# Kernel optimization log

Measured on AMD Instinct MI355X. Metric: run time of the kernel, lower is better.

## Reference

```python
import jax, jax.numpy as jnp
import numpy as np


def _l2norm(x, eps=1e-6):
    return x / jnp.sqrt(jnp.sum(x * x, axis=-1, keepdims=True) + eps)


def setup_inputs() -> dict:
    key = jax.random.key(0)
    k1, k2, k3, k4 = jax.random.split(key, 4)
    b, h, L, dk, dv = 2, 8, 4096, 128, 128
    q = jax.random.normal(k1, (b, h, L, dk), jnp.float32)
    k = jax.random.normal(k2, (b, h, L, dk), jnp.float32)
    v = jax.random.normal(k3, (b, h, L, dv), jnp.float32)
    beta = jax.random.uniform(k4, (b, h, L), jnp.float32)  # sigmoid(b_proj) in module -> (0,1)
    return {"q": q, "k": k, "v": v, "beta": beta, "chunk_size": 32}


def _delta_rule_chunkwise(q, k, v, beta, chunk_size):
    b, h, L, dk = q.shape
    dv = v.shape[-1]
    c = chunk_size
    pad = (-L) % c
    if pad:
        q = jnp.pad(q, ((0, 0), (0, 0), (0, pad), (0, 0)))
        k = jnp.pad(k, ((0, 0), (0, 0), (0, pad), (0, 0)))
        v = jnp.pad(v, ((0, 0), (0, 0), (0, pad), (0, 0)))
        beta = jnp.pad(beta, ((0, 0), (0, 0), (0, pad)))
    Lp = L + pad
    n = Lp // c

    q = _l2norm(q)
    k = _l2norm(k)
    v = v * beta[..., None]
    kb = k * beta[..., None]

    # (b,h,n,c,d)
    resh = lambda t: t.reshape(b, h, n, c, t.shape[-1])
    q, k, v, kb = resh(q), resh(k), resh(v), resh(kb)

    tri = jnp.triu(jnp.ones((c, c), bool), 0)        # upper incl diag
    tri_s = jnp.triu(jnp.ones((c, c), bool), 1)      # strict upper

    # forward substitution: inv = (I + strictly-lower(k_beta k^T))^{-1}-style recurrence
    inv = -jnp.einsum('bhncd,bhned->bhnce', kb, k)
    inv = jnp.where(tri, 0.0, inv)
    for i in range(1, c):  # fixed small chunk_size loop (c=32)
        upd = jnp.einsum('bhnk,bhnkj->bhnj', inv[..., i, :], inv[..., :, :i])
        inv = inv.at[..., i, :i].add(upd)
    inv = inv + jnp.eye(c, dtype=inv.dtype)

    u = inv @ v    # (b,h,n,c,dv)
    w = inv @ kb   # (b,h,n,c,dk)

    # chunk-recurrent state scan over the n blocks
    qs = jnp.moveaxis(q, 2, 0)
    ks = jnp.moveaxis(k, 2, 0)
    us = jnp.moveaxis(u, 2, 0)
    ws = jnp.moveaxis(w, 2, 0)
    S0 = jnp.zeros((b, h, dk, dv), q.dtype)

    def step(S, blk):
        q_i, k_i, u_i, w_i = blk
        attn = jnp.einsum('bhcd,bhed->bhce', q_i, k_i)
        attn = jnp.where(tri_s, 0.0, attn)                       # causal within chunk
        u_i = u_i - jnp.einsum('bhcd,bhde->bhce', w_i, S)
        o_i = jnp.einsum('bhcd,bhde->bhce', q_i, S) + jnp.einsum('bhce,bhed->bhcd', attn, u_i)
        S = S + jnp.einsum('bhcd,bhce->bhde', k_i, u_i)
        return S, o_i

    S, out = jax.lax.scan(step, S0, (qs, ks, us, ws))
    out = jnp.moveaxis(out, 0, 2).reshape(b, h, Lp, dv)[:, :, :L]
    return out, S


def reference(q, k, v, beta, chunk_size):
    return _delta_rule_chunkwise(q, k, v, beta, int(chunk_size))
```

## Files before the change

kernel.cpp:

```cpp
#include <hip/hip_runtime.h>
#include <cstddef>

#define BH   16
#define LSEQ 4096
#define DK   128
#define DV   128
#define C    32
#define NCH  128
#define DVB  16
#define NDVB 8
#define PP   136
#define PC   40
#define PS   136
#define AP   33

#define NPLANE (2048u * 4096u)
#define NPLAT  (2048u * 1024u)

typedef __attribute__((ext_vector_type(4))) float f32x4;
typedef __attribute__((ext_vector_type(8))) short short8;
typedef __attribute__((ext_vector_type(4))) short s16x4;

__device__ inline unsigned split_bf16(float x) {
    unsigned u = __builtin_bit_cast(unsigned, x);
    unsigned r = u + 0x7fffu + ((u >> 16) & 1u);
    unsigned h = r >> 16;
    float hf = __builtin_bit_cast(float, r & 0xffff0000u);
    float res = x - hf;
    unsigned u2 = __builtin_bit_cast(unsigned, res);
    unsigned r2 = u2 + 0x7fffu + ((u2 >> 16) & 1u);
    return (h << 16) | (r2 >> 16);
}
__device__ inline short hi_bf16(float x) {
    unsigned u = __builtin_bit_cast(unsigned, x);
    return (short)((u + 0x7fffu + ((u >> 16) & 1u)) >> 16);
}
__device__ inline short trunc_bf16(float x) {
    return (short)(__builtin_bit_cast(unsigned, x) >> 16);
}

__device__ inline short8 fld(const short* P, int row0, int pitch, int k0, int lane) {
    return *(const short8*)(P + (row0 + (lane & 15)) * pitch + k0 + ((lane >> 4) << 3));
}
__device__ inline short8 fldz128(const short* P, int row0, int ks, int lane) {
    int row = row0 + (lane & 15);
    int c = ks * 4 + (lane >> 4);
    return *(const short8*)(P + row * 128 + ((c ^ (row & 7)) << 3));
}
__device__ inline short8 fldz32(const short* P, int row0, int lane) {
    int row = row0 + (lane & 15);
    int c = lane >> 4;
    return *(const short8*)(P + row * 32 + ((c ^ (row & 3)) << 3));
}
__device__ inline f32x4 mf(short8 a, short8 b, f32x4 c) {
    return __builtin_amdgcn_mfma_f32_16x16x32_bf16(a, b, c, 0, 0, 0);
}
__device__ inline void build_ifrags(int lane, short8& Iev, short8& Iod) {
    int n = lane & 15, q = lane >> 4;
#pragma unroll
    for (int j = 0; j < 8; ++j) {
        Iev[j] = (q * 8 + j == n)      ? (short)0x3F80 : (short)0;
        Iod[j] = (q * 8 + j == n + 16) ? (short)0x3F80 : (short)0;
    }
}
__device__ inline void store8_z128(short* Pg, int row, int col0, s16x4 v) {
    int c = col0 >> 3;
    *(s16x4*)(Pg + row * 128 + ((c ^ (row & 7)) << 3) + (col0 & 7)) = v;
}
__device__ inline void store8_z32(short* Pg, int row, int col0, s16x4 v) {
    int c = col0 >> 3;
    *(s16x4*)(Pg + row * 32 + ((c ^ (row & 3)) << 3) + (col0 & 7)) = v;
}
__device__ inline void dma1k(const short* g, short* l, int lane) {
    __builtin_amdgcn_global_load_lds(
        (const __attribute__((address_space(1))) unsigned int*)(g + lane * 8),
        (__attribute__((address_space(3))) unsigned int*)l, 16, 0, 0);
}

__global__ __launch_bounds__(256) void k_prep(const float* __restrict__ Q,
                                              const float* __restrict__ K,
                                              const float* __restrict__ V,
                                              const float* __restrict__ Beta,
                                              short* __restrict__ QHg,
                                              short* __restrict__ WHg,
                                              short* __restrict__ WLg,
                                              short* __restrict__ KTHg,
                                              short* __restrict__ KTLg,
                                              short* __restrict__ ATHg,
                                              short* __restrict__ ATLg,
                                              float* __restrict__ Uws) {
    __shared__ short knh[C * PP], knl[C * PP], vh[C * PP], vl[C * PP], qh[C * PP];
    __shared__ short knTh[DK * PC], knTl[DK * PC], vTh[DK * PC], vTl[DK * PC];
    __shared__ short Th[C * PC], Tl[C * PC];
    __shared__ float A[C * AP];
    __shared__ float sbeta[C];

    const int t = threadIdx.x, lane = t & 63, wv = t >> 6;
    const int quad = (t >> 4) & 3, l15 = t & 15;
    const int g = blockIdx.x;
    const size_t base = (size_t)g * (C * DK);
    short8 Iev, Iod;
    build_ifrags(lane, Iev, Iod);

    if (t < C) sbeta[t] = Beta[(size_t)(g >> 7) * LSEQ + (size_t)(g & 127) * C + t];

    const int sr = t >> 3, sc = (t & 7) * 16;
    f32x4 kk[4], vv[4], qq[4];
#pragma unroll
    for (int g4 = 0; g4 < 4; ++g4) {
        kk[g4] = *(const f32x4*)(K + base + 16 * t + 4 * g4);
        vv[g4] = *(const f32x4*)(V + base + 16 * t + 4 * g4);
        qq[g4] = *(const f32x4*)(Q + base + 16 * t + 4 * g4);
    }
    float ssk = 0.f, ssq = 0.f;
#pragma unroll
    for (int g4 = 0; g4 < 4; ++g4) {
#pragma unroll
        for (int e = 0; e < 4; ++e) {
            ssk += kk[g4][e] * kk[g4][e];
            ssq += qq[g4][e] * qq[g4][e];
        }
    }
    ssk += __shfl_xor(ssk, 1); ssk += __shfl_xor(ssk, 2); ssk += __shfl_xor(ssk, 4);
    ssq += __shfl_xor(ssq, 1); ssq += __shfl_xor(ssq, 2); ssq += __shfl_xor(ssq, 4);
    const float rk = rsqrtf(ssk + 1e-6f), rq = rsqrtf(ssq + 1e-6f);
#pragma unroll
    for (int half = 0; half < 2; ++half) {
        short8 h8, l8;
#pragma unroll
        for (int e = 0; e < 8; ++e) {
            unsigned p = split_bf16(kk[2 * half + (e >> 2)][e & 3] * rk);
            h8[e] = (short)(p >> 16); l8[e] = (short)(p & 0xffffu);
        }
        *(short8*)(knh + sr * PP + sc + 8 * half) = h8;
        *(short8*)(knl + sr * PP + sc + 8 * half) = l8;
#pragma unroll
        for (int e = 0; e < 8; ++e) {
            unsigned p = split_bf16(vv[2 * half + (e >> 2)][e & 3]);
            h8[e] = (short)(p >> 16); l8[e] = (short)(p & 0xffffu);
        }
        *(short8*)(vh + sr * PP + sc + 8 * half) = h8;
        *(short8*)(vl + sr * PP + sc + 8 * half) = l8;
        short8 q8;
#pragma unroll
        for (int e = 0; e < 8; ++e) q8[e] = hi_bf16(qq[2 * half + (e >> 2)][e & 3] * rq);
        *(short8*)(qh + sr * PP + sc + 8 * half) = q8;
        int c = (sc >> 3) + half;
        *(short8*)(QHg + (size_t)g * 4096 + sr * 128 + ((c ^ (sr & 7)) << 3)) = q8;
    }
    __syncthreads();

    if (wv < 3) {
        const int a0 = (wv == 0) ? 0 : 16;
        const int b0 = (wv == 2) ? 16 : 0;
        f32x4 acc = {0.f, 0.f, 0.f, 0.f};
#pragma unroll
        for (int ks = 0; ks < 4; ++ks) {
            short8 ah = fld(knh, a0, PP, ks * 32, lane);
            short8 al = fld(knl, a0, PP, ks * 32, lane);
            short8 bh_ = fld(knh, b0, PP, ks * 32, lane);
            short8 bl_ = fld(knl, b0, PP, ks * 32, lane);
            acc = mf(ah, bh_, mf(ah, bl_, mf(al, bh_, acc)));
        }
#pragma unroll
        for (int r = 0; r < 4; ++r) {
            int row = a0 + quad * 4 + r, col = b0 + l15;
            A[row * AP + col] = (row > col) ? -sbeta[row] * acc[r] : 0.f;
        }
        f32x4 at = {0.f, 0.f, 0.f, 0.f};
#pragma unroll
        for (int ks = 0; ks < 4; ++ks) {
            short8 kh_ = fld(knh, b0, PP, ks * 32, lane);
            short8 kl_ = fld(knl, b0, PP, ks * 32, lane);
            short8 qf = fld(qh, a0, PP, ks * 32, lane);
            at = mf(kh_, qf, mf(kl_, qf, at));
        }
        s16x4 h4, l4;
#pragma unroll
        for (int r = 0; r < 4; ++r) {
            int cj = b0 + quad * 4 + r, ci = a0 + l15;
            float v = (cj <= ci) ? at[r] : 0.f;
            unsigned p = split_bf16(v);
            h4[r] = (short)(p >> 16); l4[r] = (short)(p & 0xffffu);
        }
        store8_z32(ATHg + (size_t)g * 1024, a0 + l15, b0 + quad * 4, h4);
        store8_z32(ATLg + (size_t)g * 1024, a0 + l15, b0 + quad * 4, l4);
    } else {
#pragma unroll
        for (int r = 0; r < 4; ++r) A[l15 * AP + 16 + quad * 4 + r] = 0.f;
        s16x4 z = {0, 0, 0, 0};
        store8_z32(ATHg + (size_t)g * 1024, l15, 16 + quad * 4, z);
        store8_z32(ATLg + (size_t)g * 1024, l15, 16 + quad * 4, z);
    }
    __syncthreads();

    auto tplane = [&](const short* src, short* dst, short* gdst) {
#pragma unroll
        for (int c0 = 0; c0 <= 16; c0 += 16) {
#pragma unroll
            for (int ks = 0; ks < 4; ++ks) {
                short8 fr = fld(src, c0, PP, ks * 32, lane);
                f32x4 z = {0.f, 0.f, 0.f, 0.f};
                f32x4 cA = mf(fr, Iev, z);
                f32x4 cB = mf(fr, Iod, z);
                s16x4 sA, sB;
#pragma unroll
                for (int r = 0; r < 4; ++r) { sA[r] = trunc_bf16(cA[r]); sB[r] = trunc_bf16(cB[r]); }
                *(s16x4*)(dst + (ks * 32 + l15) * PC + c0 + quad * 4) = sA;
                *(s16x4*)(dst + (ks * 32 + 16 + l15) * PC + c0 + quad * 4) = sB;
                if (gdst) {
                    store8_z32(gdst, ks * 32 + l15, c0 + quad * 4, sA);
                    store8_z32(gdst, ks * 32 + 16 + l15, c0 + quad * 4, sB);
                }
            }
        }
    };
    if (wv == 0) {
        tplane(knh, knTh, KTHg + (size_t)g * 4096);
        tplane(vl, vTl, nullptr);
    } else if (wv == 1) {
        tplane(knl, knTl, KTLg + (size_t)g * 4096);
    } else if (wv == 2) {
        tplane(vh, vTh, nullptr);
    } else if (lane < C) {
        const int j = lane;
        for (int i = 1; i < C; ++i) {
            float upd = 0.f;
            for (int kk2 = 1; kk2 < i; ++kk2) upd += A[i * AP + kk2] * A[kk2 * AP + j];
            if (j < i) A[i * AP + j] += upd;
        }
    }
    __syncthreads();

    {
        int tr = t >> 3, tc = (t & 7) * 4;
        s16x4 h4, l4;
#pragma unroll
        for (int e = 0; e < 4; ++e) {
            int j = tc + e;
            float val = ((tr == j) ? 1.f : (tr > j ? A[tr * AP + j] : 0.f)) * sbeta[j];
            unsigned p = split_bf16(val);
            h4[e] = (short)(p >> 16); l4[e] = (short)(p & 0xffffu);
        }
        *(s16x4*)(Th + tr * PC + tc) = h4;
        *(s16x4*)(Tl + tr * PC + tc) = l4;
    }
    __syncthreads();

    {
        const int ci0 = (wv & 1) * 16;
        short8 bTh = fld(Th, ci0, PC, 0, lane);
        short8 bTl = fld(Tl, ci0, PC, 0, lane);
        if (wv < 2) {
#pragma unroll
            for (int tt = 0; tt < 8; ++tt) {
                short8 ah = fld(vTh, tt * 16, PC, 0, lane);
                short8 al = fld(vTl, tt * 16, PC, 0, lane);
                f32x4 z = {0.f, 0.f, 0.f, 0.f};
                f32x4 acc = mf(ah, bTh, mf(ah, bTl, mf(al, bTh, z)));
                *(f32x4*)(Uws + (size_t)g * 4096 + (size_t)(ci0 + l15) * DK + tt * 16 + quad * 4) = acc;
            }
        } else {
#pragma unroll
            for (int tt = 0; tt < 8; ++tt) {
                short8 ah = fld(knTh, tt * 16, PC, 0, lane);
                short8 al = fld(knTl, tt * 16, PC, 0, lane);
                f32x4 z = {0.f, 0.f, 0.f, 0.f};
                f32x4 acc = mf(ah, bTh, mf(ah, bTl, mf(al, bTh, z)));
                s16x4 h4, l4;
#pragma unroll
                for (int r = 0; r < 4; ++r) {
                    unsigned p = split_bf16(acc[r]);
                    h4[r] = (short)(p >> 16); l4[r] = (short)(p & 0xffffu);
                }
                store8_z128(WHg + (size_t)g * 4096, ci0 + l15, tt * 16 + quad * 4, h4);
                store8_z128(WLg + (size_t)g * 4096, ci0 + l15, tt * 16 + quad * 4, l4);
            }
        }
    }
}

__global__ __launch_bounds__(512, 1) void k_scan(const short* __restrict__ QHg,
                                                 const short* __restrict__ WHg,
                                                 const short* __restrict__ WLg,
                                                 const short* __restrict__ KTHg,
                                                 const short* __restrict__ KTLg,
                                                 const short* __restrict__ ATHg,
                                                 const short* __restrict__ ATLg,
                                                 const float* __restrict__ Uws,
                                                 float* __restrict__ Out,
                                                 float* __restrict__ Sout) {
    __shared__ short bQ[2][4096], bWH[2][4096], bWL[2][4096], bKTH[2][4096], bKTL[2][4096];
    __shared__ short bATH[2][1024], bATL[2][1024];
    __shared__ short STh[DVB * PS], STl[DVB * PS];
    __shared__ short uTh[DVB * PC], uTl[DVB * PC];

    const int t = threadIdx.x, lane = t & 63, wv = t >> 6;
    const int quad = (t >> 4) & 3, l15 = t & 15;
    const int db = blockIdx.x >> 4, bhi = blockIdx.x & 15;
    const int vcol = db * DVB;
    const int r0 = (wv & 1) * 16;
    const int dk0 = wv * 16;
    const size_t gb = (size_t)bhi * NCH;

    f32x4 accS = {0.f, 0.f, 0.f, 0.f};
    float pu[4] = {0.f, 0.f, 0.f, 0.f};

    auto dma_chunk = [&](int cc, int s) {
        const size_t go = (gb + cc) * 4096;
        dma1k(QHg + go + wv * 512, &bQ[s][wv * 512], lane);
        dma1k(WHg + go + wv * 512, &bWH[s][wv * 512], lane);
        dma1k(WLg + go + wv * 512, &bWL[s][wv * 512], lane);
        dma1k(KTHg + go + wv * 512, &bKTH[s][wv * 512], lane);
        dma1k(KTLg + go + wv * 512, &bKTL[s][wv * 512], lane);
        if (wv < 4) {
            const size_t ga = (gb + cc) * 1024 + (size_t)(wv & 1) * 512;
            if (wv < 2) dma1k(ATHg + ga, &bATH[s][(wv & 1) * 512], lane);
            else        dma1k(ATLg + ga, &bATL[s][(wv & 1) * 512], lane);
        }
    };
    auto pref_u = [&](int cc) {
        if (wv < 2) {
            const size_t ub = (gb + cc) * 4096;
#pragma unroll
            for (int r = 0; r < 4; ++r)
                pu[r] = Uws[ub + (size_t)(r0 + quad * 4 + r) * DK + vcol + l15];
        }
    };

    for (int e = t; e < DVB * PS; e += 512) { STh[e] = 0; STl[e] = 0; }
    dma_chunk(0, 0);
    pref_u(0);
    __syncthreads();

    for (int cid = 0; cid < NCH; ++cid) {
        const int cur = cid & 1;
        f32x4 oc = {0.f, 0.f, 0.f, 0.f};

        if (wv < 2) {
            f32x4 u0 = {-pu[0], -pu[1], -pu[2], -pu[3]};
            f32x4 u1 = {0.f, 0.f, 0.f, 0.f}, u2 = {0.f, 0.f, 0.f, 0.f};
            f32x4 o1 = {0.f, 0.f, 0.f, 0.f};
#pragma unroll
            for (int ks = 0; ks < 4; ++ks) {
                short8 wh_ = fldz128(bWH[cur], r0, ks, lane);
                short8 wl_ = fldz128(bWL[cur], r0, ks, lane);
                short8 sh_ = fld(STh, 0, PS, ks * 32, lane);
                short8 sl_ = fld(STl, 0, PS, ks * 32, lane);
                short8 qf = fldz128(bQ[cur], r0, ks, lane);
                u0 = mf(wh_, sh_, u0);
                u1 = mf(wh_, sl_, u1);
                u2 = mf(wl_, sh_, u2);
                oc = mf(sh_, qf, oc);
                o1 = mf(sl_, qf, o1);
            }
            oc += o1;
            f32x4 us = u0 + u1 + u2;
            s16x4 h4, l4;
#pragma unroll
            for (int r = 0; r < 4; ++r) {
                unsigned p = split_bf16(-us[r]);
                h4[r] = (short)(p >> 16); l4[r] = (short)(p & 0xffffu);
            }
            *(s16x4*)(uTh + l15 * PC + r0 + quad * 4) = h4;
            *(s16x4*)(uTl + l15 * PC + r0 + quad * 4) = l4;
        }
        __syncthreads();

        short8 buh = fld(uTh, 0, PC, 0, lane);
        short8 bul = fld(uTl, 0, PC, 0, lane);
        if (wv < 2) {
            short8 bah = fldz32(bATH[cur], r0, lane);
            short8 bal = fldz32(bATL[cur], r0, lane);
            oc = mf(buh, bah, mf(buh, bal, mf(bul, bah, oc)));
            const size_t ob = ((size_t)bhi * LSEQ + (size_t)cid * C) * DK;
            *(f32x4*)(Out + ob + (size_t)(r0 + l15) * DK + vcol + quad * 4) = oc;
        }
        {
            short8 kth = fldz32(bKTH[cur], dk0, lane);
            short8 ktl = fldz32(bKTL[cur], dk0, lane);
            f32x4 z = {0.f, 0.f, 0.f, 0.f};
            f32x4 tband = mf(kth, bul, mf(ktl, buh, z));
            accS = mf(kth, buh, accS);
            accS += tband;
            s16x4 h4, l4;
#pragma unroll
            for (int r = 0; r < 4; ++r) {
                unsigned p = split_bf16(accS[r]);
                h4[r] = (short)(p >> 16); l4[r] = (short)(p & 0xffffu);
            }
            *(s16x4*)(STh + l15 * PS + dk0 + quad * 4) = h4;
            *(s16x4*)(STl + l15 * PS + dk0 + quad * 4) = l4;
        }
        if (cid + 1 < NCH) {
            dma_chunk(cid + 1, cur ^ 1);
            pref_u(cid + 1);
        }
        __syncthreads();
    }

#pragma unroll
    for (int r = 0; r < 4; ++r)
        Sout[(size_t)bhi * DK * DV + (size_t)(dk0 + quad * 4 + r) * DV + vcol + l15] = accS[r];
}

extern "C" void kernel_launch(void* const* d_in, const int* in_sizes, int n_in,
                              void* d_out, int out_size, void* d_ws, size_t ws_size,
                              hipStream_t stream) {
    const float* Q    = (const float*)d_in[0];
    const float* K    = (const float*)d_in[1];
    const float* V    = (const float*)d_in[2];
    const float* Beta = (const float*)d_in[3];

    float* Out  = (float*)d_out;
    float* Sout = Out + (size_t)BH * LSEQ * DV;

    short* QHg  = (short*)d_ws;
    short* WHg  = QHg + NPLANE;
    short* WLg  = WHg + NPLANE;
    short* KTHg = WLg + NPLANE;
    short* KTLg = KTHg + NPLANE;
    short* ATHg = KTLg + NPLANE;
    short* ATLg = ATHg + NPLAT;
    float* Uws  = (float*)(ATLg + NPLAT);

    hipLaunchKernelGGL(k_prep, dim3(BH * NCH), dim3(256), 0, stream,
                       Q, K, V, Beta, QHg, WHg, WLg, KTHg, KTLg, ATHg, ATLg, Uws);
    hipLaunchKernelGGL(k_scan, dim3(BH * NDVB), dim3(512), 0, stream,
                       QHg, WHg, WLg, KTHg, KTLg, ATHg, ATLg, Uws, Out, Sout);
}
```

Measured before the change: 356.3 us.

## Issue next-chunk DMA at loop start and defer output stores one iteration

Moves the next chunk's DMA and U prefetch to the start of each iteration so they overlap the current chunk's MFMA work. Output stores are deferred by one chunk, and the U prefetch is double-buffered in registers through a manually unrolled two-chunk loop. __syncthreads is replaced by explicit s_waitcnt plus s_barrier. The aim is to hide global-memory latency behind compute in the serial chunk scan, at the cost of more live registers and a full vmcnt wait at each iteration end.

Result: slower. 373.4 us (+4.8%).

```diff
diff --git a/kernel.cpp b/kernel.cpp
--- a/kernel.cpp
+++ b/kernel.cpp
@@ -304,7 +304,6 @@
     const size_t gb = (size_t)bhi * NCH;
 
     f32x4 accS = {0.f, 0.f, 0.f, 0.f};
-    float pu[4] = {0.f, 0.f, 0.f, 0.f};
 
     auto dma_chunk = [&](int cc, int s) {
         const size_t go = (gb + cc) * 4096;
@@ -319,26 +318,35 @@
             else        dma1k(ATLg + ga, &bATL[s][(wv & 1) * 512], lane);
         }
     };
-    auto pref_u = [&](int cc) {
+    auto pref_u = [&](int cc, f32x4& pn) {
         if (wv < 2) {
             const size_t ub = (gb + cc) * 4096;
 #pragma unroll
             for (int r = 0; r < 4; ++r)
-                pu[r] = Uws[ub + (size_t)(r0 + quad * 4 + r) * DK + vcol + l15];
+                pn[r] = Uws[ub + (size_t)(r0 + quad * 4 + r) * DK + vcol + l15];
         }
     };
 
     for (int e = t; e < DVB * PS; e += 512) { STh[e] = 0; STl[e] = 0; }
+    f32x4 puA = {0.f, 0.f, 0.f, 0.f}, puB = {0.f, 0.f, 0.f, 0.f};
+    f32x4 ocp = {0.f, 0.f, 0.f, 0.f};
     dma_chunk(0, 0);
-    pref_u(0);
+    pref_u(0, puA);
     __syncthreads();
 
-    for (int cid = 0; cid < NCH; ++cid) {
-        const int cur = cid & 1;
+    auto body = [&](int cid, int cur, f32x4& puC, f32x4& puN) {
+        if (wv < 2 && cid > 0) {
+            const size_t ob = ((size_t)bhi * LSEQ + (size_t)(cid - 1) * C) * DK;
+            *(f32x4*)(Out + ob + (size_t)(r0 + l15) * DK + vcol + quad * 4) = ocp;
+        }
+        if (cid + 1 < NCH) {
+            dma_chunk(cid + 1, cur ^ 1);
+            pref_u(cid + 1, puN);
+        }
+
         f32x4 oc = {0.f, 0.f, 0.f, 0.f};
-
         if (wv < 2) {
-            f32x4 u0 = {-pu[0], -pu[1], -pu[2], -pu[3]};
+            f32x4 u0 = {-puC[0], -puC[1], -puC[2], -puC[3]};
             f32x4 u1 = {0.f, 0.f, 0.f, 0.f}, u2 = {0.f, 0.f, 0.f, 0.f};
             f32x4 o1 = {0.f, 0.f, 0.f, 0.f};
 #pragma unroll
@@ -365,7 +373,7 @@
             *(s16x4*)(uTh + l15 * PC + r0 + quad * 4) = h4;
             *(s16x4*)(uTl + l15 * PC + r0 + quad * 4) = l4;
         }
-        __syncthreads();
+        asm volatile("s_waitcnt lgkmcnt(0)\n\ts_barrier" ::: "memory");
 
         short8 buh = fld(uTh, 0, PC, 0, lane);
         short8 bul = fld(uTl, 0, PC, 0, lane);
@@ -373,8 +381,7 @@
             short8 bah = fldz32(bATH[cur], r0, lane);
             short8 bal = fldz32(bATL[cur], r0, lane);
             oc = mf(buh, bah, mf(buh, bal, mf(bul, bah, oc)));
-            const size_t ob = ((size_t)bhi * LSEQ + (size_t)cid * C) * DK;
-            *(f32x4*)(Out + ob + (size_t)(r0 + l15) * DK + vcol + quad * 4) = oc;
+            ocp = oc;
         }
         {
             short8 kth = fldz32(bKTH[cur], dk0, lane);
@@ -392,11 +399,16 @@
             *(s16x4*)(STh + l15 * PS + dk0 + quad * 4) = h4;
             *(s16x4*)(STl + l15 * PS + dk0 + quad * 4) = l4;
         }
-        if (cid + 1 < NCH) {
-            dma_chunk(cid + 1, cur ^ 1);
-            pref_u(cid + 1);
-        }
-        __syncthreads();
+        asm volatile("s_waitcnt vmcnt(0) lgkmcnt(0)\n\ts_barrier" ::: "memory");
+    };
+
+    for (int cp = 0; cp < NCH / 2; ++cp) {
+        body(2 * cp,     0, puA, puB);
+        body(2 * cp + 1, 1, puB, puA);
+    }
+    if (wv < 2) {
+        const size_t ob = ((size_t)bhi * LSEQ + (size_t)(NCH - 1) * C) * DK;
+        *(f32x4*)(Out + ob + (size_t)(r0 + l15) * DK + vcol + quad * 4) = ocp;
     }
 
 #pragma unroll
```

## Pack per-chunk operands into contiguous records and specialize DMA warps in scan

Applied to the files above, without the earlier changes.

Replaces the seven separate global planes (Q, W hi/lo, K^T hi/lo, A^T hi/lo) with one contiguous per-chunk record, so the scan kernel can fetch each chunk as a single linear block into one unified LDS buffer. The next-chunk async copy is now issued at the start of each iteration, and only by the waves that do not compute U/O, so it overlaps with the MFMA work of waves 0-1. K^T and A^T fragment loads are hoisted ahead of the barrier. This gives better locality and earlier prefetch, but all loads land on fewer waves and the scheduling changes.

Result: faster. 339.4 us (-4.8%).

```diff
diff --git a/kernel.cpp b/kernel.cpp
--- a/kernel.cpp
+++ b/kernel.cpp
@@ -14,8 +14,14 @@
 #define PS   136
 #define AP   33
 
-#define NPLANE (2048u * 4096u)
-#define NPLAT  (2048u * 1024u)
+#define RECSZ 22528
+#define OQ    0
+#define OWH   4096
+#define OWL   8192
+#define OKTH  12288
+#define OKTL  16384
+#define OATH  20480
+#define OATL  21504
 
 typedef __attribute__((ext_vector_type(4))) float f32x4;
 typedef __attribute__((ext_vector_type(8))) short short8;
@@ -81,13 +87,7 @@
                                               const float* __restrict__ K,
                                               const float* __restrict__ V,
                                               const float* __restrict__ Beta,
-                                              short* __restrict__ QHg,
-                                              short* __restrict__ WHg,
-                                              short* __restrict__ WLg,
-                                              short* __restrict__ KTHg,
-                                              short* __restrict__ KTLg,
-                                              short* __restrict__ ATHg,
-                                              short* __restrict__ ATLg,
+                                              short* __restrict__ RECg,
                                               float* __restrict__ Uws) {
     __shared__ short knh[C * PP], knl[C * PP], vh[C * PP], vl[C * PP], qh[C * PP];
     __shared__ short knTh[DK * PC], knTl[DK * PC], vTh[DK * PC], vTl[DK * PC];
@@ -99,6 +99,7 @@
     const int quad = (t >> 4) & 3, l15 = t & 15;
     const int g = blockIdx.x;
     const size_t base = (size_t)g * (C * DK);
+    short* rec = RECg + (size_t)g * RECSZ;
     short8 Iev, Iod;
     build_ifrags(lane, Iev, Iod);
 
@@ -146,7 +147,7 @@
         for (int e = 0; e < 8; ++e) q8[e] = hi_bf16(qq[2 * half + (e >> 2)][e & 3] * rq);
         *(short8*)(qh + sr * PP + sc + 8 * half) = q8;
         int c = (sc >> 3) + half;
-        *(short8*)(QHg + (size_t)g * 4096 + sr * 128 + ((c ^ (sr & 7)) << 3)) = q8;
+        *(short8*)(rec + OQ + sr * 128 + ((c ^ (sr & 7)) << 3)) = q8;
     }
     __syncthreads();
 
@@ -183,14 +184,14 @@
             unsigned p = split_bf16(v);
             h4[r] = (short)(p >> 16); l4[r] = (short)(p & 0xffffu);
         }
-        store8_z32(ATHg + (size_t)g * 1024, a0 + l15, b0 + quad * 4, h4);
-        store8_z32(ATLg + (size_t)g * 1024, a0 + l15, b0 + quad * 4, l4);
+        store8_z32(rec + OATH, a0 + l15, b0 + quad * 4, h4);
+        store8_z32(rec + OATL, a0 + l15, b0 + quad * 4, l4);
     } else {
 #pragma unroll
         for (int r = 0; r < 4; ++r) A[l15 * AP + 16 + quad * 4 + r] = 0.f;
         s16x4 z = {0, 0, 0, 0};
-        store8_z32(ATHg + (size_t)g * 1024, l15, 16 + quad * 4, z);
-        store8_z32(ATLg + (size_t)g * 1024, l15, 16 + quad * 4, z);
+        store8_z32(rec + OATH, l15, 16 + quad * 4, z);
+        store8_z32(rec + OATL, l15, 16 + quad * 4, z);
     }
     __syncthreads();
 
@@ -216,10 +217,10 @@
         }
     };
     if (wv == 0) {
-        tplane(knh, knTh, KTHg + (size_t)g * 4096);
+        tplane(knh, knTh, rec + OKTH);
         tplane(vl, vTl, nullptr);
     } else if (wv == 1) {
-        tplane(knl, knTl, KTLg + (size_t)g * 4096);
+        tplane(knl, knTl, rec + OKTL);
     } else if (wv == 2) {
         tplane(vh, vTh, nullptr);
     } else if (lane < C) {
@@ -273,25 +274,18 @@
                     unsigned p = split_bf16(acc[r]);
                     h4[r] = (short)(p >> 16); l4[r] = (short)(p & 0xffffu);
                 }
-                store8_z128(WHg + (size_t)g * 4096, ci0 + l15, tt * 16 + quad * 4, h4);
-                store8_z128(WLg + (size_t)g * 4096, ci0 + l15, tt * 16 + quad * 4, l4);
-            }
-        }
-    }
-}
-
-__global__ __launch_bounds__(512, 1) void k_scan(const short* __restrict__ QHg,
-                                                 const short* __restrict__ WHg,
-                                                 const short* __restrict__ WLg,
-                                                 const short* __restrict__ KTHg,
-                                                 const short* __restrict__ KTLg,
-                                                 const short* __restrict__ ATHg,
-                                                 const short* __restrict__ ATLg,
+                store8_z128(rec + OWH, ci0 + l15, tt * 16 + quad * 4, h4);
+                store8_z128(rec + OWL, ci0 + l15, tt * 16 + quad * 4, l4);
+            }
+        }
+    }
+}
+
+__global__ __launch_bounds__(512, 1) void k_scan(const short* __restrict__ RECg,
                                                  const float* __restrict__ Uws,
                                                  float* __restrict__ Out,
                                                  float* __restrict__ Sout) {
-    __shared__ short bQ[2][4096], bWH[2][4096], bWL[2][4096], bKTH[2][4096], bKTL[2][4096];
-    __shared__ short bATH[2][1024], bATL[2][1024];
+    __shared__ __attribute__((aligned(16))) short bALL[2][RECSZ];
     __shared__ short STh[DVB * PS], STl[DVB * PS];
     __shared__ short uTh[DVB * PC], uTl[DVB * PC];
 
@@ -307,16 +301,13 @@
     float pu[4] = {0.f, 0.f, 0.f, 0.f};
 
     auto dma_chunk = [&](int cc, int s) {
-        const size_t go = (gb + cc) * 4096;
-        dma1k(QHg + go + wv * 512, &bQ[s][wv * 512], lane);
-        dma1k(WHg + go + wv * 512, &bWH[s][wv * 512], lane);
-        dma1k(WLg + go + wv * 512, &bWL[s][wv * 512], lane);
-        dma1k(KTHg + go + wv * 512, &bKTH[s][wv * 512], lane);
-        dma1k(KTLg + go + wv * 512, &bKTL[s][wv * 512], lane);
-        if (wv < 4) {
-            const size_t ga = (gb + cc) * 1024 + (size_t)(wv & 1) * 512;
-            if (wv < 2) dma1k(ATHg + ga, &bATH[s][(wv & 1) * 512], lane);
-            else        dma1k(ATLg + ga, &bATL[s][(wv & 1) * 512], lane);
+        if (wv < 2) return;
+        const short* src = RECg + (size_t)(gb + cc) * RECSZ;
+        short* dst = bALL[s];
+#pragma unroll
+        for (int k = 0; k < 8; ++k) {
+            int q = (wv - 2) + 6 * k;
+            if (q < 44) dma1k(src + q * 512, dst + q * 512, lane);
         }
     };
     auto pref_u = [&](int cc) {
@@ -335,19 +326,29 @@
 
     for (int cid = 0; cid < NCH; ++cid) {
         const int cur = cid & 1;
+        const short* pC = bALL[cur];
         f32x4 oc = {0.f, 0.f, 0.f, 0.f};
 
-        if (wv < 2) {
-            f32x4 u0 = {-pu[0], -pu[1], -pu[2], -pu[3]};
+        short8 kth = fldz32(pC + OKTH, dk0, lane);
+        short8 ktl = fldz32(pC + OKTL, dk0, lane);
+        short8 bah = {}, bal = {};
+
+        if (wv >= 2) {
+            if (cid + 1 < NCH) dma_chunk(cid + 1, cur ^ 1);
+        } else {
+            float p0 = pu[0], p1 = pu[1], p2 = pu[2], p3 = pu[3];
+            if (cid + 1 < NCH) pref_u(cid + 1);
+
+            f32x4 u0 = {-p0, -p1, -p2, -p3};
             f32x4 u1 = {0.f, 0.f, 0.f, 0.f}, u2 = {0.f, 0.f, 0.f, 0.f};
             f32x4 o1 = {0.f, 0.f, 0.f, 0.f};
 #pragma unroll
             for (int ks = 0; ks < 4; ++ks) {
-                short8 wh_ = fldz128(bWH[cur], r0, ks, lane);
-                short8 wl_ = fldz128(bWL[cur], r0, ks, lane);
+                short8 wh_ = fldz128(pC + OWH, r0, ks, lane);
+                short8 wl_ = fldz128(pC + OWL, r0, ks, lane);
                 short8 sh_ = fld(STh, 0, PS, ks * 32, lane);
                 short8 sl_ = fld(STl, 0, PS, ks * 32, lane);
-                short8 qf = fldz128(bQ[cur], r0, ks, lane);
+                short8 qf = fldz128(pC + OQ, r0, ks, lane);
                 u0 = mf(wh_, sh_, u0);
                 u1 = mf(wh_, sl_, u1);
                 u2 = mf(wl_, sh_, u2);
@@ -364,21 +365,19 @@
             }
             *(s16x4*)(uTh + l15 * PC + r0 + quad * 4) = h4;
             *(s16x4*)(uTl + l15 * PC + r0 + quad * 4) = l4;
+            bah = fldz32(pC + OATH, r0, lane);
+            bal = fldz32(pC + OATL, r0, lane);
         }
         __syncthreads();
 
         short8 buh = fld(uTh, 0, PC, 0, lane);
         short8 bul = fld(uTl, 0, PC, 0, lane);
         if (wv < 2) {
-            short8 bah = fldz32(bATH[cur], r0, lane);
-            short8 bal = fldz32(bATL[cur], r0, lane);
             oc = mf(buh, bah, mf(buh, bal, mf(bul, bah, oc)));
             const size_t ob = ((size_t)bhi * LSEQ + (size_t)cid * C) * DK;
             *(f32x4*)(Out + ob + (size_t)(r0 + l15) * DK + vcol + quad * 4) = oc;
         }
         {
-            short8 kth = fldz32(bKTH[cur], dk0, lane);
-            short8 ktl = fldz32(bKTL[cur], dk0, lane);
             f32x4 z = {0.f, 0.f, 0.f, 0.f};
             f32x4 tband = mf(kth, bul, mf(ktl, buh, z));
             accS = mf(kth, buh, accS);
@@ -391,10 +390,6 @@
             }
             *(s16x4*)(STh + l15 * PS + dk0 + quad * 4) = h4;
             *(s16x4*)(STl + l15 * PS + dk0 + quad * 4) = l4;
-        }
-        if (cid + 1 < NCH) {
-            dma_chunk(cid + 1, cur ^ 1);
-            pref_u(cid + 1);
         }
         __syncthreads();
     }
@@ -415,17 +410,11 @@
     float* Out  = (float*)d_out;
     float* Sout = Out + (size_t)BH * LSEQ * DV;
 
-    short* QHg  = (short*)d_ws;
-    short* WHg  = QHg + NPLANE;
-    short* WLg  = WHg + NPLANE;
-    short* KTHg = WLg + NPLANE;
-    short* KTLg = KTHg + NPLANE;
-    short* ATHg = KTLg + NPLANE;
-    short* ATLg = ATHg + NPLAT;
-    float* Uws  = (float*)(ATLg + NPLAT);
+    short* RECg = (short*)d_ws;
+    float* Uws  = (float*)(RECg + (size_t)BH * NCH * RECSZ);
 
     hipLaunchKernelGGL(k_prep, dim3(BH * NCH), dim3(256), 0, stream,
-                       Q, K, V, Beta, QHg, WHg, WLg, KTHg, KTLg, ATHg, ATLg, Uws);
+                       Q, K, V, Beta, RECg, Uws);
     hipLaunchKernelGGL(k_scan, dim3(BH * NDVB), dim3(512), 0, stream,
-                       QHg, WHg, WLg, KTHg, KTLg, ATHg, ATLg, Uws, Out, Sout);
-}
+                       RECg, Uws, Out, Sout);
+}
```
